# Kernel tuning notes

Measured on AMD Instinct MI355X. Metric: run time of the kernel, lower is better.

Reference implementation:

```python
import jax, jax.numpy as jnp
import numpy as np

N = 50000       # nodes
E = 800000      # edges (avg degree 16)
H = 64          # hidden_channels
L = 4           # num_layers
EPS_MSG = 1e-7  # GENConv message eps
EPS_SM = 1e-16  # PyG softmax denominator eps
LN_EPS = 1e-5   # torch LayerNorm eps


def layer_norm(x, g, b):
    mu = jnp.mean(x, axis=-1, keepdims=True)
    var = jnp.mean((x - mu) ** 2, axis=-1, keepdims=True)
    return (x - mu) / jnp.sqrt(var + LN_EPS) * g + b


def gen_conv(x, src, dst, t, W1, b1, mg, mb, W2, b2):
    # message: relu(x_j) + eps, shape [E, H]
    msg = jax.nn.relu(x[src]) + EPS_MSG
    # per-destination, per-channel softmax over incoming edges of msg * t
    w = msg * t
    mx = jax.ops.segment_max(w, dst, num_segments=N)           # [N, H]
    ex = jnp.exp(w - mx[dst])                                  # [E, H]
    sm = jax.ops.segment_sum(ex, dst, num_segments=N)          # [N, H]
    alpha = ex / (sm[dst] + EPS_SM)
    agg = jax.ops.segment_sum(msg * alpha, dst, num_segments=N)
    out = agg + x                                              # root (x_r) add
    # MLP [H -> 2H -> H] with LayerNorm + ReLU after first linear
    h = out @ W1.T + b1
    h = jax.nn.relu(layer_norm(h, mg, mb))
    return h @ W2.T + b2


def setup_inputs() -> dict:
    key = jax.random.key(0)
    k = jax.random.split(key, 4)
    x = jax.random.normal(k[0], (N, H), jnp.float32)
    edge_index = jax.random.randint(k[1], (2, E), 0, N, jnp.int32)
    kw = jax.random.split(k[2], 2)
    W1 = jax.random.normal(kw[0], (L, 2 * H, H), jnp.float32) * 0.05
    W2 = jax.random.normal(kw[1], (L, H, 2 * H), jnp.float32) * 0.05
    return dict(
        x=x,
        edge_index=edge_index,
        t=jnp.ones((L,), jnp.float32),                 # learn_t, init 1.0
        W1=W1,
        b1=jnp.zeros((L, 2 * H), jnp.float32),
        mg=jnp.ones((L, 2 * H), jnp.float32),          # GENConv MLP LayerNorm gamma
        mb=jnp.zeros((L, 2 * H), jnp.float32),
        W2=W2,
        b2=jnp.zeros((L, H), jnp.float32),
        lng=jnp.ones((L, H), jnp.float32),             # DeepGCNLayer LayerNorm gamma
        lnb=jnp.zeros((L, H), jnp.float32),
    )


def reference(x, edge_index, t, W1, b1, mg, mb, W2, b2, lng, lnb):
    src, dst = edge_index[0], edge_index[1]
    # layers[0].conv applied raw
    x = gen_conv(x, src, dst, t[0], W1[0], b1[0], mg[0], mb[0], W2[0], b2[0])
    # res+ blocks: x + conv(act(norm(x)))  (dropout is identity in eval)
    for i in range(1, L):
        h = jax.nn.relu(layer_norm(x, lng[i], lnb[i]))
        x = x + gen_conv(h, src, dst, t[i], W1[i], b1[i], mg[i], mb[i], W2[i], b2[i])
    # final: layers[0].act(layers[0].norm(x)) (dropout identity in eval)
    return jax.nn.relu(layer_norm(x, lng[0], lnb[0]))
```

## Files before the change

kernel.cpp:

```cpp
#include <hip/hip_runtime.h>
#include <hip/hip_bf16.h>


typedef unsigned int uint;
typedef __attribute__((ext_vector_type(8))) short bf16x8;
typedef __attribute__((ext_vector_type(4))) float f32x4;

static __device__ __forceinline__ float wave_sum(float v) {
    #pragma unroll
    for (int o = 32; o; o >>= 1) v += __shfl_xor(v, o);
    return v;
}

static __device__ __forceinline__ uint f2bf(float f) {
    uint u = __builtin_bit_cast(uint, f);
    return (u + 0x7FFFu + ((u >> 16) & 1u)) >> 16;
}

static __device__ __forceinline__ uint4 pk4(float4 a, float4 b) {
    uint4 p;
    p.x = f2bf(a.x) | (f2bf(a.y) << 16);
    p.y = f2bf(a.z) | (f2bf(a.w) << 16);
    p.z = f2bf(b.x) | (f2bf(b.y) << 16);
    p.w = f2bf(b.z) | (f2bf(b.w) << 16);
    return p;
}

union FragU { uint4 u; bf16x8 v; };

#define EPB 4096
#define BCAP 4096

__global__ void zero_bcnt_k(int* __restrict__ p) { p[threadIdx.x] = 0; }

__global__ __launch_bounds__(256) void bucket_scatter_k(const int* __restrict__ src,
                                                        const int* __restrict__ dst,
                                                        int* __restrict__ bcnt,
                                                        int2* __restrict__ stage, int e) {
    __shared__ int lcnt[512];
    __shared__ int lbase[512];
    __shared__ int rkbuf[EPB];
    int tid = threadIdx.x;
    for (int i = tid; i < 512; i += 256) lcnt[i] = 0;
    __syncthreads();
    int i0 = blockIdx.x * EPB;
    int cnt = min(EPB, e - i0);
    for (int k = tid; k < cnt; k += 256) {
        int d = dst[i0 + k];
        rkbuf[k] = atomicAdd(&lcnt[d >> 7], 1);
    }
    __syncthreads();
    for (int i = tid; i < 512; i += 256)
        lbase[i] = lcnt[i] ? atomicAdd(&bcnt[i], lcnt[i]) : 0;
    __syncthreads();
    for (int k = tid; k < cnt; k += 256) {
        int s = src[i0 + k];
        int d = dst[i0 + k];
        int b = d >> 7;
        stage[(size_t)b * BCAP + lbase[b] + rkbuf[k]] = make_int2(s, d);
    }
}

__global__ __launch_bounds__(256) void bucket_to_csr_k(const int2* __restrict__ stage,
                                                       const int* __restrict__ bcnt,
                                                       int* __restrict__ csr,
                                                       int* __restrict__ offs,
                                                       int* __restrict__ deg, int n) {
    __shared__ int lcnt[128];
    __shared__ int loff[128];
    __shared__ int wl[128];
    int b = blockIdx.x;
    int tid = threadIdx.x;
    int base = b << 7;
    if (tid < 128) lcnt[tid] = 0;
    __syncthreads();
    int cnt = bcnt[b];
    const int2* sb = stage + (size_t)b * BCAP;
    for (int k = tid; k < cnt; k += 256)
        atomicAdd(&lcnt[sb[k].y & 127], 1);
    __syncthreads();
    if (tid < 128) loff[tid] = lcnt[tid];
    __syncthreads();
    #pragma unroll
    for (int o = 1; o < 128; o <<= 1) {
        int v = 0;
        if (tid < 128 && tid >= o) v = loff[tid - o];
        __syncthreads();
        if (tid < 128) loff[tid] += v;
        __syncthreads();
    }
    if (tid < 128) {
        int ex = loff[tid] - lcnt[tid];
        wl[tid] = ex;
        if (base + tid < n) {
            offs[base + tid] = b * BCAP + ex;
            deg[base + tid] = lcnt[tid];
        }
    }
    __syncthreads();
    for (int k = tid; k < cnt; k += 256) {
        int2 sd = sb[k];
        int slot = atomicAdd(&wl[sd.y & 127], 1);
        csr[(size_t)b * BCAP + slot] = sd.x;
    }
}

__global__ __launch_bounds__(256) void conv_k(const float* __restrict__ h,
                                              const int* __restrict__ offs,
                                              const int* __restrict__ deg,
                                              const int* __restrict__ csr,
                                              const float* __restrict__ tptr,
                                              float* __restrict__ out, int n) {
    int wid = threadIdx.x >> 6, lane = threadIdx.x & 63;
    int node = blockIdx.x * 4 + wid;
    if (node >= n) return;
    float tt = tptr[0];
    int start = offs[node], d = deg[node];
    float m = -__builtin_huge_valf(), num = 0.f, den = 0.f;
    int i = 0;
    for (; i + 8 <= d; i += 8) {
        int sx[8];
        float v[8];
        #pragma unroll
        for (int q = 0; q < 8; q++) sx[q] = csr[start + i + q];
        #pragma unroll
        for (int q = 0; q < 8; q++) v[q] = h[(size_t)sx[q] * 64 + lane];
        float msg[8], w[8];
        float wm = m;
        #pragma unroll
        for (int q = 0; q < 8; q++) {
            msg[q] = fmaxf(v[q], 0.f) + 1e-7f;
            w[q] = msg[q] * tt;
            wm = fmaxf(wm, w[q]);
        }
        float sc = __expf(m - wm);
        num *= sc; den *= sc;
        #pragma unroll
        for (int q = 0; q < 8; q++) {
            float p = __expf(w[q] - wm);
            num += msg[q] * p;
            den += p;
        }
        m = wm;
    }
    for (; i + 4 <= d; i += 4) {
        int s0 = csr[start + i],     s1 = csr[start + i + 1];
        int s2 = csr[start + i + 2], s3 = csr[start + i + 3];
        float v0 = h[(size_t)s0 * 64 + lane];
        float v1 = h[(size_t)s1 * 64 + lane];
        float v2 = h[(size_t)s2 * 64 + lane];
        float v3 = h[(size_t)s3 * 64 + lane];
        float msg0 = fmaxf(v0, 0.f) + 1e-7f;
        float msg1 = fmaxf(v1, 0.f) + 1e-7f;
        float msg2 = fmaxf(v2, 0.f) + 1e-7f;
        float msg3 = fmaxf(v3, 0.f) + 1e-7f;
        float w0 = msg0 * tt, w1 = msg1 * tt, w2 = msg2 * tt, w3 = msg3 * tt;
        float nm = fmaxf(fmaxf(m, fmaxf(w0, w1)), fmaxf(w2, w3));
        float sc = __expf(m - nm);
        float p0 = __expf(w0 - nm), p1 = __expf(w1 - nm);
        float p2 = __expf(w2 - nm), p3 = __expf(w3 - nm);
        num = num * sc + (msg0 * p0 + msg1 * p1) + (msg2 * p2 + msg3 * p3);
        den = den * sc + (p0 + p1) + (p2 + p3);
        m = nm;
    }
    for (; i < d; i++) {
        int s0 = csr[start + i];
        float v0 = h[(size_t)s0 * 64 + lane];
        float msg0 = fmaxf(v0, 0.f) + 1e-7f;
        float w0 = msg0 * tt;
        float nm = fmaxf(m, w0);
        float sc = __expf(m - nm);
        float p0 = __expf(w0 - nm);
        num = num * sc + msg0 * p0;
        den = den * sc + p0;
        m = nm;
    }
    float agg = num / (den + 1e-16f);
    out[(size_t)node * 64 + lane] = agg + h[(size_t)node * 64 + lane];
}

template <int RES, int WX>
__global__ __launch_bounds__(256) void mlp_fused_k(
        const float* __restrict__ zin,
        const float* __restrict__ W1, const float* __restrict__ b1,
        const float* __restrict__ mg, const float* __restrict__ mb,
        const float* __restrict__ W2, const float* __restrict__ b2,
        const float* __restrict__ g2, const float* __restrict__ bb2,
        float* __restrict__ xio, float* __restrict__ hout, int n) {
    __shared__ uint lw1[16 * 64 * 4];
    __shared__ uint lw2[16 * 64 * 4];
    __shared__ uint lrt[4 * 1024];
    __shared__ float sp[576];
    int tid = threadIdx.x;
    int wid = tid >> 6, lane = tid & 63;
    int nodeL = lane & 15, g = lane >> 4;

    #pragma unroll
    for (int q = 0; q < 4; q++) {
        int f = wid * 4 + q;
        int jt = f >> 1, ks = f & 1;
        const float* s = W1 + (jt * 16 + nodeL) * 64 + ks * 32 + g * 8;
        float4 a = *(const float4*)s, b = *(const float4*)(s + 4);
        *(uint4*)&lw1[(f * 64 + lane) * 4] = pk4(a, b);
    }
    #pragma unroll
    for (int q = 0; q < 4; q++) {
        int f = wid * 4 + q;
        int ct = f >> 2, ks = f & 3;
        const float* s = W2 + (ct * 16 + nodeL) * 128 + ks * 32 + g * 8;
        float4 a = *(const float4*)s, b = *(const float4*)(s + 4);
        *(uint4*)&lw2[(f * 64 + lane) * 4] = pk4(a, b);
    }
    if (tid < 128) { sp[tid] = b1[tid]; sp[128 + tid] = mg[tid]; sp[256 + tid] = mb[tid]; }
    else if (tid < 192) {
        int i = tid - 128;
        sp[384 + i] = b2[i]; sp[448 + i] = g2[i]; sp[512 + i] = bb2[i];
    }
    __syncthreads();

    uint* rt = lrt + wid * 1024;
    int nt = (n + 15) >> 4;
    for (int tile = blockIdx.x * 4 + wid; tile < nt; tile += gridDim.x * 4) {
        int node = tile * 16 + nodeL;
        int rnode = min(node, n - 1);
        const float* zp = zin + (size_t)rnode * 64 + g * 8;
        float4 z0 = *(const float4*)zp,        z1 = *(const float4*)(zp + 4);
        float4 z2 = *(const float4*)(zp + 32), z3 = *(const float4*)(zp + 36);
        FragU zb0, zb1;
        zb0.u = pk4(z0, z1);
        zb1.u = pk4(z2, z3);

        f32x4 acc[8];
        #pragma unroll
        for (int jt = 0; jt < 8; jt++) {
            FragU wA, wB;
            wA.u = *(const uint4*)&lw1[((jt * 2 + 0) * 64 + lane) * 4];
            wB.u = *(const uint4*)&lw1[((jt * 2 + 1) * 64 + lane) * 4];
            f32x4 c = {0.f, 0.f, 0.f, 0.f};
            c = __builtin_amdgcn_mfma_f32_16x16x32_bf16(wA.v, zb0.v, c, 0, 0, 0);
            c = __builtin_amdgcn_mfma_f32_16x16x32_bf16(wB.v, zb1.v, c, 0, 0, 0);
            acc[jt] = c;
        }
        float s1 = 0.f, s2 = 0.f;
        float h[8][4];
        #pragma unroll
        for (int jt = 0; jt < 8; jt++)
            #pragma unroll
            for (int jj = 0; jj < 4; jj++) {
                float v = acc[jt][jj] + sp[jt * 16 + 4 * g + jj];
                h[jt][jj] = v; s1 += v; s2 += v * v;
            }
        s1 += __shfl_xor(s1, 16); s1 += __shfl_xor(s1, 32);
        s2 += __shfl_xor(s2, 16); s2 += __shfl_xor(s2, 32);
        float mu = s1 * (1.f / 128.f);
        float var = s2 * (1.f / 128.f) - mu * mu;
        float rstd = rsqrtf(fmaxf(var, 0.f) + 1e-5f);
        #pragma unroll
        for (int jt = 0; jt < 8; jt++)
            #pragma unroll
            for (int jp = 0; jp < 2; jp++) {
                int j0 = jt * 16 + 4 * g + 2 * jp;
                float r0 = fmaxf((h[jt][2 * jp] - mu) * rstd * sp[128 + j0] + sp[256 + j0], 0.f);
                float r1 = fmaxf((h[jt][2 * jp + 1] - mu) * rstd * sp[128 + j0 + 1] + sp[256 + j0 + 1], 0.f);
                uint val = f2bf(r0) | (f2bf(r1) << 16);
                uint byte = (uint)(nodeL * 256 + jt * 32 + g * 8 + jp * 4) ^ ((uint)nodeL << 4);
                rt[byte >> 2] = val;
            }
        FragU rb[4];
        #pragma unroll
        for (int ks = 0; ks < 4; ks++) {
            uint byte = (uint)(nodeL * 256 + ks * 64 + g * 16) ^ ((uint)nodeL << 4);
            rb[ks].u = *(const uint4*)((const char*)rt + byte);
        }
        f32x4 acc2[4];
        #pragma unroll
        for (int ct = 0; ct < 4; ct++) {
            f32x4 c = {0.f, 0.f, 0.f, 0.f};
            #pragma unroll
            for (int ks = 0; ks < 4; ks++) {
                FragU wf;
                wf.u = *(const uint4*)&lw2[((ct * 4 + ks) * 64 + lane) * 4];
                c = __builtin_amdgcn_mfma_f32_16x16x32_bf16(wf.v, rb[ks].v, c, 0, 0, 0);
            }
            acc2[ct] = c;
        }
        if (node < n) {
            float o[4][4];
            float t1 = 0.f, t2 = 0.f;
            #pragma unroll
            for (int ct = 0; ct < 4; ct++) {
                float4 res;
                if (RES) res = *(const float4*)(xio + (size_t)node * 64 + ct * 16 + 4 * g);
                #pragma unroll
                for (int jj = 0; jj < 4; jj++) {
                    float v = acc2[ct][jj] + sp[384 + ct * 16 + 4 * g + jj];
                    if (RES) v += ((const float*)&res)[jj];
                    o[ct][jj] = v; t1 += v; t2 += v * v;
                }
                if (WX) *(float4*)(xio + (size_t)node * 64 + ct * 16 + 4 * g) =
                    make_float4(o[ct][0], o[ct][1], o[ct][2], o[ct][3]);
            }
            t1 += __shfl_xor(t1, 16); t1 += __shfl_xor(t1, 32);
            t2 += __shfl_xor(t2, 16); t2 += __shfl_xor(t2, 32);
            float mu2 = t1 * (1.f / 64.f);
            float var2 = t2 * (1.f / 64.f) - mu2 * mu2;
            float rs2 = rsqrtf(fmaxf(var2, 0.f) + 1e-5f);
            #pragma unroll
            for (int ct = 0; ct < 4; ct++) {
                float4 ov;
                #pragma unroll
                for (int jj = 0; jj < 4; jj++) {
                    int co = ct * 16 + 4 * g + jj;
                    ((float*)&ov)[jj] =
                        fmaxf((o[ct][jj] - mu2) * rs2 * sp[448 + co] + sp[512 + co], 0.f);
                }
                *(float4*)(hout + (size_t)node * 64 + ct * 16 + 4 * g) = ov;
            }
        }
    }
}

extern "C" void kernel_launch(void* const* d_in, const int* in_sizes, int n_in,
                              void* d_out, int out_size, void* d_ws, size_t ws_size,
                              hipStream_t stream) {
    const float* x   = (const float*)d_in[0];
    const int*   ei  = (const int*)d_in[1];
    const float* t   = (const float*)d_in[2];
    const float* W1  = (const float*)d_in[3];
    const float* b1  = (const float*)d_in[4];
    const float* mg  = (const float*)d_in[5];
    const float* mb  = (const float*)d_in[6];
    const float* W2  = (const float*)d_in[7];
    const float* b2  = (const float*)d_in[8];
    const float* lng = (const float*)d_in[9];
    const float* lnb = (const float*)d_in[10];

    int n = in_sizes[0] / 64;
    int e = in_sizes[1] / 2;
    const int* src = ei;
    const int* dst = ei + e;

    char* ws = (char*)d_ws;
    size_t off = 0;
    auto alloc = [&](size_t bytes) -> void* {
        void* p = ws + off;
        off = (off + bytes + 255) & ~(size_t)255;
        return p;
    };
    int*   bcnt  = (int*)alloc(512 * 4);
    int*   offs  = (int*)alloc((size_t)n * 4);
    int*   deg   = (int*)alloc((size_t)n * 4);
    int*   csr   = (int*)alloc((size_t)512 * BCAP * 4);
    float* xcur  = (float*)alloc((size_t)n * 64 * 4);
    float* hin   = (float*)alloc((size_t)n * 64 * 4);
    float* tmp   = (float*)alloc((size_t)n * 64 * 4);
    int2*  stage = (int2*)alloc((size_t)512 * BCAP * 8);

    int nbuck = (n + 127) >> 7;
    zero_bcnt_k<<<1, 512, 0, stream>>>(bcnt);
    bucket_scatter_k<<<(e + EPB - 1) / EPB, 256, 0, stream>>>(src, dst, bcnt, stage, e);
    bucket_to_csr_k<<<nbuck, 256, 0, stream>>>(stage, bcnt, csr, offs, deg, n);

    int nodeBlocks = (n + 3) / 4;
    const int mlpGrid = 512;

    conv_k<<<nodeBlocks, 256, 0, stream>>>(x, offs, deg, csr, t + 0, tmp, n);
    mlp_fused_k<0, 1><<<mlpGrid, 256, 0, stream>>>(tmp, W1, b1, mg, mb, W2, b2,
                                                   lng + 64, lnb + 64, xcur, hin, n);
    for (int i = 1; i <= 2; i++) {
        conv_k<<<nodeBlocks, 256, 0, stream>>>(hin, offs, deg, csr, t + i, tmp, n);
        mlp_fused_k<1, 1><<<mlpGrid, 256, 0, stream>>>(
            tmp, W1 + (size_t)i * 8192, b1 + i * 128, mg + i * 128, mb + i * 128,
            W2 + (size_t)i * 8192, b2 + i * 64,
            lng + (i + 1) * 64, lnb + (i + 1) * 64, xcur, hin, n);
    }
    conv_k<<<nodeBlocks, 256, 0, stream>>>(hin, offs, deg, csr, t + 3, tmp, n);
    mlp_fused_k<1, 0><<<mlpGrid, 256, 0, stream>>>(
        tmp, W1 + (size_t)3 * 8192, b1 + 3 * 128, mg + 3 * 128, mb + 3 * 128,
        W2 + (size_t)3 * 8192, b2 + 3 * 64, lng, lnb, xcur, (float*)d_out, n);
}
```

Measured before the change: 332.4 us.

## Store gathered node features and conv outputs in bf16 to halve gather traffic

Result: faster. 320.6 us (-3.6%).

```diff
diff --git a/kernel.cpp b/kernel.cpp
--- a/kernel.cpp
+++ b/kernel.cpp
@@ -3,20 +3,17 @@
 
 
 typedef unsigned int uint;
+typedef unsigned short ushort;
 typedef __attribute__((ext_vector_type(8))) short bf16x8;
 typedef __attribute__((ext_vector_type(4))) float f32x4;
-
-static __device__ __forceinline__ float wave_sum(float v) {
-    #pragma unroll
-    for (int o = 32; o; o >>= 1) v += __shfl_xor(v, o);
-    return v;
-}
 
 static __device__ __forceinline__ uint f2bf(float f) {
     uint u = __builtin_bit_cast(uint, f);
     return (u + 0x7FFFu + ((u >> 16) & 1u)) >> 16;
 }
-
+static __device__ __forceinline__ float bf2f(uint u) {
+    return __builtin_bit_cast(float, u << 16);
+}
 static __device__ __forceinline__ uint4 pk4(float4 a, float4 b) {
     uint4 p;
     p.x = f2bf(a.x) | (f2bf(a.y) << 16);
@@ -32,6 +29,16 @@
 #define BCAP 4096
 
 __global__ void zero_bcnt_k(int* __restrict__ p) { p[threadIdx.x] = 0; }
+
+__global__ void cast_k(const float* __restrict__ in, ushort* __restrict__ out, int n4) {
+    int g = blockIdx.x * blockDim.x + threadIdx.x;
+    if (g < n4) {
+        float4 v = ((const float4*)in)[g];
+        ushort4 o;
+        o.x = f2bf(v.x); o.y = f2bf(v.y); o.z = f2bf(v.z); o.w = f2bf(v.w);
+        ((ushort4*)out)[g] = o;
+    }
+}
 
 __global__ __launch_bounds__(256) void bucket_scatter_k(const int* __restrict__ src,
                                                         const int* __restrict__ dst,
@@ -105,12 +112,12 @@
     }
 }
 
-__global__ __launch_bounds__(256) void conv_k(const float* __restrict__ h,
+__global__ __launch_bounds__(256) void conv_k(const ushort* __restrict__ h,
                                               const int* __restrict__ offs,
                                               const int* __restrict__ deg,
                                               const int* __restrict__ csr,
                                               const float* __restrict__ tptr,
-                                              float* __restrict__ out, int n) {
+                                              ushort* __restrict__ out, int n) {
     int wid = threadIdx.x >> 6, lane = threadIdx.x & 63;
     int node = blockIdx.x * 4 + wid;
     if (node >= n) return;
@@ -124,7 +131,7 @@
         #pragma unroll
         for (int q = 0; q < 8; q++) sx[q] = csr[start + i + q];
         #pragma unroll
-        for (int q = 0; q < 8; q++) v[q] = h[(size_t)sx[q] * 64 + lane];
+        for (int q = 0; q < 8; q++) v[q] = bf2f(h[(size_t)sx[q] * 64 + lane]);
         float msg[8], w[8];
         float wm = m;
         #pragma unroll
@@ -146,10 +153,10 @@
     for (; i + 4 <= d; i += 4) {
         int s0 = csr[start + i],     s1 = csr[start + i + 1];
         int s2 = csr[start + i + 2], s3 = csr[start + i + 3];
-        float v0 = h[(size_t)s0 * 64 + lane];
-        float v1 = h[(size_t)s1 * 64 + lane];
-        float v2 = h[(size_t)s2 * 64 + lane];
-        float v3 = h[(size_t)s3 * 64 + lane];
+        float v0 = bf2f(h[(size_t)s0 * 64 + lane]);
+        float v1 = bf2f(h[(size_t)s1 * 64 + lane]);
+        float v2 = bf2f(h[(size_t)s2 * 64 + lane]);
+        float v3 = bf2f(h[(size_t)s3 * 64 + lane]);
         float msg0 = fmaxf(v0, 0.f) + 1e-7f;
         float msg1 = fmaxf(v1, 0.f) + 1e-7f;
         float msg2 = fmaxf(v2, 0.f) + 1e-7f;
@@ -165,7 +172,7 @@
     }
     for (; i < d; i++) {
         int s0 = csr[start + i];
-        float v0 = h[(size_t)s0 * 64 + lane];
+        float v0 = bf2f(h[(size_t)s0 * 64 + lane]);
         float msg0 = fmaxf(v0, 0.f) + 1e-7f;
         float w0 = msg0 * tt;
         float nm = fmaxf(m, w0);
@@ -176,17 +183,19 @@
         m = nm;
     }
     float agg = num / (den + 1e-16f);
-    out[(size_t)node * 64 + lane] = agg + h[(size_t)node * 64 + lane];
-}
-
-template <int RES, int WX>
+    float hn = bf2f(h[(size_t)node * 64 + lane]);
+    out[(size_t)node * 64 + lane] = (ushort)f2bf(agg + hn);
+}
+
+template <int RES, int FINAL>
 __global__ __launch_bounds__(256) void mlp_fused_k(
-        const float* __restrict__ zin,
+        const ushort* __restrict__ zin,
         const float* __restrict__ W1, const float* __restrict__ b1,
         const float* __restrict__ mg, const float* __restrict__ mb,
         const float* __restrict__ W2, const float* __restrict__ b2,
         const float* __restrict__ g2, const float* __restrict__ bb2,
-        float* __restrict__ xio, float* __restrict__ hout, int n) {
+        float* __restrict__ xio, ushort* __restrict__ houtb,
+        float* __restrict__ houtf, int n) {
     __shared__ uint lw1[16 * 64 * 4];
     __shared__ uint lw2[16 * 64 * 4];
     __shared__ uint lrt[4 * 1024];
@@ -223,12 +232,10 @@
     for (int tile = blockIdx.x * 4 + wid; tile < nt; tile += gridDim.x * 4) {
         int node = tile * 16 + nodeL;
         int rnode = min(node, n - 1);
-        const float* zp = zin + (size_t)rnode * 64 + g * 8;
-        float4 z0 = *(const float4*)zp,        z1 = *(const float4*)(zp + 4);
-        float4 z2 = *(const float4*)(zp + 32), z3 = *(const float4*)(zp + 36);
+        const ushort* zp = zin + (size_t)rnode * 64;
         FragU zb0, zb1;
-        zb0.u = pk4(z0, z1);
-        zb1.u = pk4(z2, z3);
+        zb0.u = *(const uint4*)(zp + g * 8);
+        zb1.u = *(const uint4*)(zp + 32 + g * 8);
 
         f32x4 acc[8];
         #pragma unroll
@@ -297,7 +304,7 @@
                     if (RES) v += ((const float*)&res)[jj];
                     o[ct][jj] = v; t1 += v; t2 += v * v;
                 }
-                if (WX) *(float4*)(xio + (size_t)node * 64 + ct * 16 + 4 * g) =
+                if (!FINAL) *(float4*)(xio + (size_t)node * 64 + ct * 16 + 4 * g) =
                     make_float4(o[ct][0], o[ct][1], o[ct][2], o[ct][3]);
             }
             t1 += __shfl_xor(t1, 16); t1 += __shfl_xor(t1, 32);
@@ -307,14 +314,18 @@
             float rs2 = rsqrtf(fmaxf(var2, 0.f) + 1e-5f);
             #pragma unroll
             for (int ct = 0; ct < 4; ct++) {
-                float4 ov;
-                #pragma unroll
-                for (int jj = 0; jj < 4; jj++) {
-                    int co = ct * 16 + 4 * g + jj;
-                    ((float*)&ov)[jj] =
-                        fmaxf((o[ct][jj] - mu2) * rs2 * sp[448 + co] + sp[512 + co], 0.f);
+                float ln0 = fmaxf((o[ct][0] - mu2) * rs2 * sp[448 + ct * 16 + 4 * g + 0] + sp[512 + ct * 16 + 4 * g + 0], 0.f);
+                float ln1 = fmaxf((o[ct][1] - mu2) * rs2 * sp[448 + ct * 16 + 4 * g + 1] + sp[512 + ct * 16 + 4 * g + 1], 0.f);
+                float ln2 = fmaxf((o[ct][2] - mu2) * rs2 * sp[448 + ct * 16 + 4 * g + 2] + sp[512 + ct * 16 + 4 * g + 2], 0.f);
+                float ln3 = fmaxf((o[ct][3] - mu2) * rs2 * sp[448 + ct * 16 + 4 * g + 3] + sp[512 + ct * 16 + 4 * g + 3], 0.f);
+                if (FINAL) {
+                    *(float4*)(houtf + (size_t)node * 64 + ct * 16 + 4 * g) =
+                        make_float4(ln0, ln1, ln2, ln3);
+                } else {
+                    ushort4 ov;
+                    ov.x = f2bf(ln0); ov.y = f2bf(ln1); ov.z = f2bf(ln2); ov.w = f2bf(ln3);
+                    *(ushort4*)(houtb + (size_t)node * 64 + ct * 16 + 4 * g) = ov;
                 }
-                *(float4*)(hout + (size_t)node * 64 + ct * 16 + 4 * g) = ov;
             }
         }
     }
@@ -347,35 +358,37 @@
         off = (off + bytes + 255) & ~(size_t)255;
         return p;
     };
-    int*   bcnt  = (int*)alloc(512 * 4);
-    int*   offs  = (int*)alloc((size_t)n * 4);
-    int*   deg   = (int*)alloc((size_t)n * 4);
-    int*   csr   = (int*)alloc((size_t)512 * BCAP * 4);
-    float* xcur  = (float*)alloc((size_t)n * 64 * 4);
-    float* hin   = (float*)alloc((size_t)n * 64 * 4);
-    float* tmp   = (float*)alloc((size_t)n * 64 * 4);
-    int2*  stage = (int2*)alloc((size_t)512 * BCAP * 8);
+    int*    bcnt  = (int*)alloc(512 * 4);
+    int*    offs  = (int*)alloc((size_t)n * 4);
+    int*    deg   = (int*)alloc((size_t)n * 4);
+    int*    csr   = (int*)alloc((size_t)512 * BCAP * 4);
+    float*  xcur  = (float*)alloc((size_t)n * 64 * 4);
+    ushort* xb    = (ushort*)alloc((size_t)n * 64 * 2);
+    ushort* hb    = (ushort*)alloc((size_t)n * 64 * 2);
+    ushort* tmpb  = (ushort*)alloc((size_t)n * 64 * 2);
+    int2*   stage = (int2*)alloc((size_t)512 * BCAP * 8);
 
     int nbuck = (n + 127) >> 7;
     zero_bcnt_k<<<1, 512, 0, stream>>>(bcnt);
     bucket_scatter_k<<<(e + EPB - 1) / EPB, 256, 0, stream>>>(src, dst, bcnt, stage, e);
     bucket_to_csr_k<<<nbuck, 256, 0, stream>>>(stage, bcnt, csr, offs, deg, n);
+    cast_k<<<(n * 16 + 255) / 256, 256, 0, stream>>>(x, xb, n * 16);
 
     int nodeBlocks = (n + 3) / 4;
     const int mlpGrid = 512;
 
-    conv_k<<<nodeBlocks, 256, 0, stream>>>(x, offs, deg, csr, t + 0, tmp, n);
-    mlp_fused_k<0, 1><<<mlpGrid, 256, 0, stream>>>(tmp, W1, b1, mg, mb, W2, b2,
-                                                   lng + 64, lnb + 64, xcur, hin, n);
+    conv_k<<<nodeBlocks, 256, 0, stream>>>(xb, offs, deg, csr, t + 0, tmpb, n);
+    mlp_fused_k<0, 0><<<mlpGrid, 256, 0, stream>>>(tmpb, W1, b1, mg, mb, W2, b2,
+                                                   lng + 64, lnb + 64, xcur, hb, nullptr, n);
     for (int i = 1; i <= 2; i++) {
-        conv_k<<<nodeBlocks, 256, 0, stream>>>(hin, offs, deg, csr, t + i, tmp, n);
-        mlp_fused_k<1, 1><<<mlpGrid, 256, 0, stream>>>(
-            tmp, W1 + (size_t)i * 8192, b1 + i * 128, mg + i * 128, mb + i * 128,
+        conv_k<<<nodeBlocks, 256, 0, stream>>>(hb, offs, deg, csr, t + i, tmpb, n);
+        mlp_fused_k<1, 0><<<mlpGrid, 256, 0, stream>>>(
+            tmpb, W1 + (size_t)i * 8192, b1 + i * 128, mg + i * 128, mb + i * 128,
             W2 + (size_t)i * 8192, b2 + i * 64,
-            lng + (i + 1) * 64, lnb + (i + 1) * 64, xcur, hin, n);
-    }
-    conv_k<<<nodeBlocks, 256, 0, stream>>>(hin, offs, deg, csr, t + 3, tmp, n);
-    mlp_fused_k<1, 0><<<mlpGrid, 256, 0, stream>>>(
-        tmp, W1 + (size_t)3 * 8192, b1 + 3 * 128, mg + 3 * 128, mb + 3 * 128,
-        W2 + (size_t)3 * 8192, b2 + 3 * 64, lng, lnb, xcur, (float*)d_out, n);
-}
+            lng + (i + 1) * 64, lnb + (i + 1) * 64, xcur, hb, nullptr, n);
+    }
+    conv_k<<<nodeBlocks, 256, 0, stream>>>(hb, offs, deg, csr, t + 3, tmpb, n);
+    mlp_fused_k<1, 1><<<mlpGrid, 256, 0, stream>>>(
+        tmpb, W1 + (size_t)3 * 8192, b1 + 3 * 128, mg + 3 * 128, mb + 3 * 128,
+        W2 + (size_t)3 * 8192, b2 + 3 * 64, lng, lnb, xcur, nullptr, (float*)d_out, n);
+}
```
